# Kernel tuning notes

Hardware: AMD Instinct MI355X
Metric: run time of the kernel (lower is better)

## Reference

```python
import jax, jax.numpy as jnp
import numpy as np

INPUT_SIZE = 2048
HIDDEN_SIZE = 2048
BATCH = 4096


def setup_inputs() -> dict:
    key = jax.random.key(0)
    ks = jax.random.split(key, 12)
    std = 1.0 / HIDDEN_SIZE ** 0.5
    def u(k, shape):
        return jax.random.uniform(k, shape, jnp.float32, -std, std)
    inp = {
        "x": jax.random.normal(ks[0], (BATCH, INPUT_SIZE), jnp.float32),
        "h": jax.random.normal(ks[1], (BATCH, HIDDEN_SIZE), jnp.float32),
        "c": jax.random.normal(ks[2], (BATCH, HIDDEN_SIZE), jnp.float32),
        "weight_ii": u(ks[3], (HIDDEN_SIZE, INPUT_SIZE)),
        "weight_if": u(ks[4], (HIDDEN_SIZE, INPUT_SIZE)),
        "weight_ig": u(ks[5], (HIDDEN_SIZE, INPUT_SIZE)),
        "weight_io": u(ks[6], (HIDDEN_SIZE, INPUT_SIZE)),
        "weight_hi": u(ks[7], (HIDDEN_SIZE, HIDDEN_SIZE)),
        "weight_hf": u(ks[8], (HIDDEN_SIZE, HIDDEN_SIZE)),
        "weight_hg": u(ks[9], (HIDDEN_SIZE, HIDDEN_SIZE)),
        "weight_ho": u(ks[10], (HIDDEN_SIZE, HIDDEN_SIZE)),
        "bias_i": u(ks[11], (HIDDEN_SIZE,)),
        "bias_f": u(jax.random.fold_in(key, 100), (HIDDEN_SIZE,)),
        "bias_g": u(jax.random.fold_in(key, 101), (HIDDEN_SIZE,)),
        "bias_o": u(jax.random.fold_in(key, 102), (HIDDEN_SIZE,)),
    }
    return inp


def reference(x, h, c, weight_ii, weight_if, weight_ig, weight_io,
              weight_hi, weight_hf, weight_hg, weight_ho,
              bias_i, bias_f, bias_g, bias_o):
    # Fuse the 4 input projections and 4 hidden projections into 2 GEMMs
    # (same math as 8 separate matmuls in the original module).
    W_x = jnp.concatenate([weight_ii, weight_if, weight_ig, weight_io], axis=0)  # [4H, I]
    W_h = jnp.concatenate([weight_hi, weight_hf, weight_hg, weight_ho], axis=0)  # [4H, H]
    b = jnp.concatenate([bias_i, bias_f, bias_g, bias_o], axis=0)                # [4H]
    gates = x @ W_x.T + h @ W_h.T + b                                            # [B, 4H]
    gi, gf, gg, go = jnp.split(gates, 4, axis=1)
    i = jax.nn.sigmoid(gi)
    f = jax.nn.sigmoid(gf)
    g = jnp.tanh(gg)
    o = jax.nn.sigmoid(go)
    c_new = f * c + i * g
    h_new = o * jnp.tanh(c_new)
    return (h_new, c_new)
```

## Files before the change

kernel.cpp:

```cpp
#include <hip/hip_runtime.h>
#include <cstdint>
#include <cstddef>

#define BATCH 4096
#define HID   2048
#define NT    64

typedef __attribute__((ext_vector_type(8))) short bf16x8;
typedef __attribute__((ext_vector_type(4))) float f32x4;

__device__ __forceinline__ unsigned short f2bf(float f) {
  union { float f; unsigned u; } a; a.f = f;
  unsigned u = a.u;
  return (unsigned short)((u + 0x7FFFu + ((u >> 16) & 1u)) >> 16);
}

__device__ __forceinline__ void gload_lds16(const void* g, void* l) {
  __builtin_amdgcn_global_load_lds((const __attribute__((address_space(1))) void*)g,
                                   (__attribute__((address_space(3))) void*)l, 16, 0, 0);
}

#define SCHED0() __builtin_amdgcn_sched_barrier(0)
#define SBAR()  do { SCHED0(); __builtin_amdgcn_s_barrier(); SCHED0(); } while (0)
#define WAITV(N) do { SCHED0(); asm volatile("s_waitcnt vmcnt(" #N ")" ::: "memory"); SCHED0(); } while (0)
#define WAITL(N) do { SCHED0(); asm volatile("s_waitcnt lgkmcnt(" #N ")" ::: "memory"); SCHED0(); } while (0)
#define DSR(dst, adr, IMM) asm volatile("ds_read_b128 %0, %1 offset:" #IMM : "=v"(dst) : "v"(adr))

#define RD_A2_LO(ADR) do { DSR(a2[0],ADR,4096); DSR(a2[1],ADR,5120); DSR(a2[2],ADR,6144); DSR(a2[3],ADR,7168); } while (0)
#define RD_A2_HI(ADR) do { DSR(a2[0],ADR,36864); DSR(a2[1],ADR,37888); DSR(a2[2],ADR,38912); DSR(a2[3],ADR,39936); } while (0)
#define RD_N_LO(AADR,BADR,A1,BF) do { \
  DSR(A1[0],AADR,0); DSR(A1[1],AADR,1024); DSR(A1[2],AADR,2048); DSR(A1[3],AADR,3072); \
  DSR(BF[0],BADR,0); DSR(BF[1],BADR,1024); DSR(BF[2],BADR,2048); DSR(BF[3],BADR,3072); } while (0)
#define RD_N_HI(AADR,BADR,A1,BF) do { \
  DSR(A1[0],AADR,32768); DSR(A1[1],AADR,33792); DSR(A1[2],AADR,34816); DSR(A1[3],AADR,35840); \
  DSR(BF[0],BADR,32768); DSR(BF[1],BADR,33792); DSR(BF[2],BADR,34816); DSR(BF[3],BADR,35840); } while (0)

#define MFMA_LO(A1, BF) do { _Pragma("unroll") \
  for (int m_ = 0; m_ < 4; m_++) { _Pragma("unroll") \
    for (int n_ = 0; n_ < 4; n_++) \
      acc[m_][n_] = __builtin_amdgcn_mfma_f32_16x16x32_bf16(A1[m_], BF[n_], acc[m_][n_], 0, 0, 0); } } while (0)
#define MFMA_HI(BF) do { _Pragma("unroll") \
  for (int m_ = 0; m_ < 4; m_++) { _Pragma("unroll") \
    for (int n_ = 0; n_ < 4; n_++) \
      acc[4+m_][n_] = __builtin_amdgcn_mfma_f32_16x16x32_bf16(a2[m_], BF[n_], acc[4+m_][n_], 0, 0, 0); } } while (0)

#define STAGE_G(KOFF, DOF) do { \
  gload_lds16(pA + (KOFF), dA + (DOF)); \
  gload_lds16(pA + 128*4096 + (KOFF), dA + (DOF) + 8192); \
  gload_lds16(pB + (KOFF), dA + (DOF) + 16384); \
  gload_lds16(pB + 32*4096 + (KOFF), dA + (DOF) + 16384 + 8192); } while (0)

#define SLOT(TOPV, RDA2CALL, RDNCALL, STAGECALL, MA1, MBF) do { \
  TOPV; SBAR(); WAITL(0); \
  RDA2CALL; \
  RDNCALL; \
  STAGECALL; \
  SCHED0(); \
  __builtin_amdgcn_s_setprio(1); MFMA_LO(MA1, MBF); __builtin_amdgcn_s_setprio(0); \
  WAITL(8); \
  __builtin_amdgcn_s_setprio(1); MFMA_HI(MBF); __builtin_amdgcn_s_setprio(0); \
} while (0)

__global__ __launch_bounds__(256) void convert_kernel(
    const float* __restrict__ x, const float* __restrict__ h,
    const float* __restrict__ wii, const float* __restrict__ wif,
    const float* __restrict__ wig, const float* __restrict__ wio,
    const float* __restrict__ whi, const float* __restrict__ whf,
    const float* __restrict__ whg, const float* __restrict__ who,
    unsigned short* __restrict__ Abf, unsigned short* __restrict__ Wbf) {
  int seg = blockIdx.y;
  const float* src;
  unsigned short* dst;
  int ofs;
  size_t rofs;
  if (seg < 4) {
    src = (seg < 2) ? x : h;
    dst = Abf;
    ofs = (seg < 2) ? 0 : 2048;
    rofs = (seg & 1) ? 2048 : 0;
    src += rofs * 2048;
  } else {
    int g = (seg - 4) & 3;
    dst = Wbf + (size_t)g * 2048 * 4096;
    ofs = (seg >= 8) ? 2048 : 0;
    rofs = 0;
    switch (seg) {
      case 4: src = wii; break; case 5: src = wif; break;
      case 6: src = wig; break; case 7: src = wio; break;
      case 8: src = whi; break; case 9: src = whf; break;
      case 10: src = whg; break; default: src = who; break;
    }
  }
  size_t idx = (size_t)blockIdx.x * 256 + threadIdx.x;
  size_t e = idx * 4;
  int n = (int)(e >> 11);
  int k = (int)(e & 2047);
  float4 v = *(const float4*)(src + e);
  ushort4 o;
  o.x = f2bf(v.x); o.y = f2bf(v.y); o.z = f2bf(v.z); o.w = f2bf(v.w);
  *(ushort4*)(dst + (rofs + (size_t)n) * 4096 + ofs + k) = o;
}

__global__ __launch_bounds__(512, 2) void lstm_gemm8(
    const unsigned short* __restrict__ Abf, const unsigned short* __restrict__ Wbf,
    const float* __restrict__ c_in,
    const float* __restrict__ bias_i, const float* __restrict__ bias_f,
    const float* __restrict__ bias_g, const float* __restrict__ bias_o,
    float* __restrict__ out) {
  __shared__ unsigned short lds[2][4][256 * 32];

  int tid = threadIdx.x;
  int lane = tid & 63;
  int wid = tid >> 6;
  int wr = wid >> 2;
  int wc = wid & 3;
  int lrow = lane & 15;
  int qh = lane >> 4;

  int bid = blockIdx.x;
  int xcd = bid & 7;
  int t7 = bid >> 3;
  int mt = t7 & 15;
  int bn = xcd * 4 + (t7 >> 4);
  int m0 = mt * 256;

  int r0 = tid >> 2, cc0 = tid & 3;
  int ccs0 = cc0 ^ ((r0 >> 1) & 3);
  const unsigned short* pA = Abf + (size_t)(m0 + r0) * 4096 + ccs0 * 8;
  int g0 = (r0 >> 4) & 3;
  int jw = bn * 64 + ((r0 >> 6) & 3) * 16 + (r0 & 15);
  const unsigned short* pB = Wbf + ((size_t)g0 * 2048 + jw) * 4096 + ccs0 * 8;

  char* L0 = (char*)&lds[0][0][0];
  char* dA = L0 + tid * 16;
  unsigned ldsOff = (unsigned)(size_t)(__attribute__((address_space(3))) char*)L0;

  int arow0 = wr * 128 + lrow;
  int brow0 = wc * 64 + lrow;
  unsigned qsA = ((unsigned)(qh ^ ((arow0 >> 1) & 3))) << 4;
  unsigned qsB = ((unsigned)(qh ^ ((brow0 >> 1) & 3))) << 4;
  unsigned a0 = ldsOff + (unsigned)arow0 * 64 + qsA;
  unsigned b0 = ldsOff + 16384u + (unsigned)brow0 * 64 + qsB;
  unsigned a1v = a0 + 65536u;
  unsigned b1v = b0 + 65536u;

  f32x4 acc[8][4];
  #pragma unroll
  for (int a = 0; a < 8; a++)
    #pragma unroll
    for (int b = 0; b < 4; b++) acc[a][b] = (f32x4){0.f, 0.f, 0.f, 0.f};

  bf16x8 a1A[4], bfA[4], a1B[4], bfB[4], a2[4];

  STAGE_G(0, 0);
  STAGE_G(32, 32768);
  STAGE_G(64, 65536);
  WAITV(8);
  SBAR();
  RD_N_LO(a0, b0, a1A, bfA);

  for (int i = 0; i < 31; ++i) {
    int kb = i * 128;
    SLOT(WAITV(4), RD_A2_LO(a0), RD_N_HI(a0, b0, a1B, bfB), STAGE_G(kb + 96, 98304), a1A, bfA);
    SLOT(WAITV(4), RD_A2_HI(a0), RD_N_LO(a1v, b1v, a1A, bfA), STAGE_G(kb + 128, 0), a1B, bfB);
    SLOT(WAITV(4), RD_A2_LO(a1v), RD_N_HI(a1v, b1v, a1B, bfB), STAGE_G(kb + 160, 32768), a1A, bfA);
    SLOT(WAITV(4), RD_A2_HI(a1v), RD_N_LO(a0, b0, a1A, bfA), STAGE_G(kb + 192, 65536), a1B, bfB);
  }

  SLOT(WAITV(4), RD_A2_LO(a0), RD_N_HI(a0, b0, a1B, bfB), STAGE_G(4064, 98304), a1A, bfA);
  SLOT(WAITV(4), RD_A2_HI(a0), RD_N_LO(a1v, b1v, a1A, bfA), (void)0, a1B, bfB);
  SLOT(WAITV(0), RD_A2_LO(a1v), RD_N_HI(a1v, b1v, a1B, bfB), (void)0, a1A, bfA);
  WAITL(0);
  RD_A2_HI(a1v);
  SCHED0();
  __builtin_amdgcn_s_setprio(1); MFMA_LO(a1B, bfB); __builtin_amdgcn_s_setprio(0);
  WAITL(0);
  __builtin_amdgcn_s_setprio(1); MFMA_HI(bfB); __builtin_amdgcn_s_setprio(0);

  int j = bn * 64 + wc * 16 + lrow;
  float bi = bias_i[j], bff = bias_f[j], bgg = bias_g[j], bo = bias_o[j];
  int rbase = m0 + wr * 128 + qh * 4;
  #pragma unroll
  for (int mf = 0; mf < 8; mf++) {
    #pragma unroll
    for (int qq = 0; qq < 4; qq++) {
      int m = rbase + mf * 16 + qq;
      size_t off = (size_t)m * HID + j;
      float gi = acc[mf][0][qq] + bi;
      float gf = acc[mf][1][qq] + bff;
      float gg = acc[mf][2][qq] + bgg;
      float go = acc[mf][3][qq] + bo;
      float iv = 1.f / (1.f + __expf(-gi));
      float fv = 1.f / (1.f + __expf(-gf));
      float gv = tanhf(gg);
      float ov = 1.f / (1.f + __expf(-go));
      float cn = fv * c_in[off] + iv * gv;
      float hn = ov * tanhf(cn);
      out[off] = hn;
      out[(size_t)BATCH * HID + off] = cn;
    }
  }
}

__global__ __launch_bounds__(256) void lstm_gemm_fb(
    const float* __restrict__ x, const float* __restrict__ h,
    const float* __restrict__ wii, const float* __restrict__ wif,
    const float* __restrict__ wig, const float* __restrict__ wio,
    const float* __restrict__ whi, const float* __restrict__ whf,
    const float* __restrict__ whg, const float* __restrict__ who,
    const float* __restrict__ c_in,
    const float* __restrict__ bias_i, const float* __restrict__ bias_f,
    const float* __restrict__ bias_g, const float* __restrict__ bias_o,
    float* __restrict__ out) {
  __shared__ unsigned short Ald[128 * 64];
  __shared__ unsigned short Bld[128 * 64];
  int tid = threadIdx.x;
  int lane = tid & 63;
  int wid = tid >> 6;
  int wr = wid >> 1, wc = wid & 1;
  int bid = blockIdx.x;
  int swz = (bid & 7) * 256 + (bid >> 3);
  int mt = swz & 31;
  int ht = swz >> 5;
  int m0 = mt * 128;
  int j0 = ht * 32;
  f32x4 acc[4][4];
  #pragma unroll
  for (int a = 0; a < 4; a++)
    #pragma unroll
    for (int b = 0; b < 4; b++) acc[a][b] = (f32x4){0.f, 0.f, 0.f, 0.f};
  int lrow = lane & 15;
  int lsw = lrow & 7;
  int qbase = lane >> 4;
  for (int kt = 0; kt < 64; kt++) {
    int k0 = kt * 64;
    const float* Asrc = (k0 < 2048) ? x : h;
    int ka = k0 & 2047;
    #pragma unroll
    for (int i = 0; i < 4; i++) {
      int c = i * 256 + tid;
      int r = c >> 3, cc = c & 7;
      int ccs = cc ^ (r & 7);
      const float* s = Asrc + (size_t)(m0 + r) * 2048 + ka + ccs * 8;
      float4 v0 = *(const float4*)s;
      float4 v1 = *(const float4*)(s + 4);
      bf16x8 pk;
      pk[0] = (short)f2bf(v0.x); pk[1] = (short)f2bf(v0.y);
      pk[2] = (short)f2bf(v0.z); pk[3] = (short)f2bf(v0.w);
      pk[4] = (short)f2bf(v1.x); pk[5] = (short)f2bf(v1.y);
      pk[6] = (short)f2bf(v1.z); pk[7] = (short)f2bf(v1.w);
      *(bf16x8*)((char*)Ald + (size_t)c * 16) = pk;
    }
    #pragma unroll
    for (int i = 0; i < 4; i++) {
      int c = i * 256 + tid;
      int rb = c >> 3, cc = c & 7;
      int ccs = cc ^ (rb & 7);
      int g = rb >> 5, jj = rb & 31;
      const float* Bsrc;
      if (k0 < 2048) Bsrc = (g == 0) ? wii : (g == 1) ? wif : (g == 2) ? wig : wio;
      else           Bsrc = (g == 0) ? whi : (g == 1) ? whf : (g == 2) ? whg : who;
      const float* s = Bsrc + (size_t)(j0 + jj) * 2048 + ka + ccs * 8;
      float4 v0 = *(const float4*)s;
      float4 v1 = *(const float4*)(s + 4);
      bf16x8 pk;
      pk[0] = (short)f2bf(v0.x); pk[1] = (short)f2bf(v0.y);
      pk[2] = (short)f2bf(v0.z); pk[3] = (short)f2bf(v0.w);
      pk[4] = (short)f2bf(v1.x); pk[5] = (short)f2bf(v1.y);
      pk[6] = (short)f2bf(v1.z); pk[7] = (short)f2bf(v1.w);
      *(bf16x8*)((char*)Bld + (size_t)c * 16) = pk;
    }
    __syncthreads();
    #pragma unroll
    for (int ks = 0; ks < 2; ks++) {
      int q = ks * 4 + qbase;
      int qs8 = (q ^ lsw) * 8;
      bf16x8 af[4], bg[4];
      #pragma unroll
      for (int mf = 0; mf < 4; mf++)
        af[mf] = *(const bf16x8*)&Ald[(wr * 64 + mf * 16 + lrow) * 64 + qs8];
      #pragma unroll
      for (int g = 0; g < 4; g++)
        bg[g] = *(const bf16x8*)&Bld[(g * 32 + wc * 16 + lrow) * 64 + qs8];
      #pragma unroll
      for (int mf = 0; mf < 4; mf++)
        #pragma unroll
        for (int g = 0; g < 4; g++)
          acc[mf][g] = __builtin_amdgcn_mfma_f32_16x16x32_bf16(af[mf], bg[g], acc[mf][g], 0, 0, 0);
    }
    __syncthreads();
  }
  int j = j0 + wc * 16 + lrow;
  float bi = bias_i[j], bff = bias_f[j], bgg = bias_g[j], bo = bias_o[j];
  int rbase = m0 + wr * 64 + (lane >> 4) * 4;
  #pragma unroll
  for (int mf = 0; mf < 4; mf++) {
    #pragma unroll
    for (int q = 0; q < 4; q++) {
      int m = rbase + mf * 16 + q;
      size_t off = (size_t)m * HID + j;
      float gi = acc[mf][0][q] + bi;
      float gf = acc[mf][1][q] + bff;
      float gg = acc[mf][2][q] + bgg;
      float go = acc[mf][3][q] + bo;
      float iv = 1.f / (1.f + __expf(-gi));
      float fv = 1.f / (1.f + __expf(-gf));
      float gv = tanhf(gg);
      float ov = 1.f / (1.f + __expf(-go));
      float cn = fv * c_in[off] + iv * gv;
      float hn = ov * tanhf(cn);
      out[off] = hn;
      out[(size_t)BATCH * HID + off] = cn;
    }
  }
}

extern "C" void kernel_launch(void* const* d_in, const int* in_sizes, int n_in,
                              void* d_out, int out_size, void* d_ws, size_t ws_size,
                              hipStream_t stream) {
  const float* x   = (const float*)d_in[0];
  const float* h   = (const float*)d_in[1];
  const float* c   = (const float*)d_in[2];
  const float* wii = (const float*)d_in[3];
  const float* wif = (const float*)d_in[4];
  const float* wig = (const float*)d_in[5];
  const float* wio = (const float*)d_in[6];
  const float* whi = (const float*)d_in[7];
  const float* whf = (const float*)d_in[8];
  const float* whg = (const float*)d_in[9];
  const float* who = (const float*)d_in[10];
  const float* bi  = (const float*)d_in[11];
  const float* bf  = (const float*)d_in[12];
  const float* bg  = (const float*)d_in[13];
  const float* bo  = (const float*)d_in[14];
  float* out = (float*)d_out;

  size_t needA = (size_t)4096 * 4096 * 2;
  size_t needW = (size_t)8192 * 4096 * 2;

  if (ws_size >= needA + needW) {
    unsigned short* Abf = (unsigned short*)d_ws;
    unsigned short* Wbf = (unsigned short*)((char*)d_ws + needA);
    convert_kernel<<<dim3(4096, 12), 256, 0, stream>>>(
        x, h, wii, wif, wig, wio, whi, whf, whg, who, Abf, Wbf);
    lstm_gemm8<<<512, 512, 0, stream>>>(Abf, Wbf, c, bi, bf, bg, bo, out);
  } else {
    lstm_gemm_fb<<<2048, 256, 0, stream>>>(
        x, h, wii, wif, wig, wio, whi, whf, whg, who,
        c, bi, bf, bg, bo, out);
  }
}
```

Measured before the change: 315.7 us.

## Deepen LDS pipeline to five rotating stages with runtime offset ring

Replaces the fixed two-buffer, hi/lo-halved LDS layout with a five-slot ring buffer of 32 KB stages whose offsets rotate at runtime. Four K-chunks are prefetched up front, and each slot now waits with a looser vmcnt, so more global loads are in flight during the MFMA work. The cost is more LDS (160 KB), which may reduce occupancy below two blocks per CU. Runtime offset arithmetic also replaces the immediate-offset addressing, adding extra scalar and vector ALU work.

After: 321.2 us. Within noise of the previous version (+1.7%).

```diff
diff --git a/kernel.cpp b/kernel.cpp
--- a/kernel.cpp
+++ b/kernel.cpp
@@ -4,7 +4,6 @@
 
 #define BATCH 4096
 #define HID   2048
-#define NT    64
 
 typedef __attribute__((ext_vector_type(8))) short bf16x8;
 typedef __attribute__((ext_vector_type(4))) float f32x4;
@@ -26,14 +25,10 @@
 #define WAITL(N) do { SCHED0(); asm volatile("s_waitcnt lgkmcnt(" #N ")" ::: "memory"); SCHED0(); } while (0)
 #define DSR(dst, adr, IMM) asm volatile("ds_read_b128 %0, %1 offset:" #IMM : "=v"(dst) : "v"(adr))
 
-#define RD_A2_LO(ADR) do { DSR(a2[0],ADR,4096); DSR(a2[1],ADR,5120); DSR(a2[2],ADR,6144); DSR(a2[3],ADR,7168); } while (0)
-#define RD_A2_HI(ADR) do { DSR(a2[0],ADR,36864); DSR(a2[1],ADR,37888); DSR(a2[2],ADR,38912); DSR(a2[3],ADR,39936); } while (0)
-#define RD_N_LO(AADR,BADR,A1,BF) do { \
+#define RD_A2(ADR) do { DSR(a2[0],ADR,4096); DSR(a2[1],ADR,5120); DSR(a2[2],ADR,6144); DSR(a2[3],ADR,7168); } while (0)
+#define RD_N(AADR,BADR,A1,BF) do { \
   DSR(A1[0],AADR,0); DSR(A1[1],AADR,1024); DSR(A1[2],AADR,2048); DSR(A1[3],AADR,3072); \
   DSR(BF[0],BADR,0); DSR(BF[1],BADR,1024); DSR(BF[2],BADR,2048); DSR(BF[3],BADR,3072); } while (0)
-#define RD_N_HI(AADR,BADR,A1,BF) do { \
-  DSR(A1[0],AADR,32768); DSR(A1[1],AADR,33792); DSR(A1[2],AADR,34816); DSR(A1[3],AADR,35840); \
-  DSR(BF[0],BADR,32768); DSR(BF[1],BADR,33792); DSR(BF[2],BADR,34816); DSR(BF[3],BADR,35840); } while (0)
 
 #define MFMA_LO(A1, BF) do { _Pragma("unroll") \
   for (int m_ = 0; m_ < 4; m_++) { _Pragma("unroll") \
@@ -48,17 +43,21 @@
   gload_lds16(pA + (KOFF), dA + (DOF)); \
   gload_lds16(pA + 128*4096 + (KOFF), dA + (DOF) + 8192); \
   gload_lds16(pB + (KOFF), dA + (DOF) + 16384); \
-  gload_lds16(pB + 32*4096 + (KOFF), dA + (DOF) + 16384 + 8192); } while (0)
-
-#define SLOT(TOPV, RDA2CALL, RDNCALL, STAGECALL, MA1, MBF) do { \
-  TOPV; SBAR(); WAITL(0); \
-  RDA2CALL; \
-  RDNCALL; \
-  STAGECALL; \
-  SCHED0(); \
+  gload_lds16(pB + 32*4096 + (KOFF), dA + (DOF) + 24576); } while (0)
+
+#define ADVR(o) do { (o) += 32768; if ((o) == 163840) (o) = 0; } while (0)
+
+#define SLOT(VN, SA, SB, STG, MA1, MBF) do { \
+  WAITV(VN); \
+  SBAR(); \
+  { unsigned aC_ = aBase + (unsigned)o_c; RD_A2(aC_); } \
+  { unsigned aN_ = aBase + (unsigned)o_n, bN_ = bBase + (unsigned)o_n; RD_N(aN_, bN_, SA, SB); } \
+  STG; \
+  WAITL(12); \
   __builtin_amdgcn_s_setprio(1); MFMA_LO(MA1, MBF); __builtin_amdgcn_s_setprio(0); \
   WAITL(8); \
   __builtin_amdgcn_s_setprio(1); MFMA_HI(MBF); __builtin_amdgcn_s_setprio(0); \
+  ADVR(o_c); ADVR(o_n); ADVR(o_s); koff += 32; \
 } while (0)
 
 __global__ __launch_bounds__(256) void convert_kernel(
@@ -107,7 +106,7 @@
     const float* __restrict__ bias_i, const float* __restrict__ bias_f,
     const float* __restrict__ bias_g, const float* __restrict__ bias_o,
     float* __restrict__ out) {
-  __shared__ unsigned short lds[2][4][256 * 32];
+  __shared__ unsigned short lds[5 * 16384];
 
   int tid = threadIdx.x;
   int lane = tid & 63;
@@ -131,7 +130,7 @@
   int jw = bn * 64 + ((r0 >> 6) & 3) * 16 + (r0 & 15);
   const unsigned short* pB = Wbf + ((size_t)g0 * 2048 + jw) * 4096 + ccs0 * 8;
 
-  char* L0 = (char*)&lds[0][0][0];
+  char* L0 = (char*)&lds[0];
   char* dA = L0 + tid * 16;
   unsigned ldsOff = (unsigned)(size_t)(__attribute__((address_space(3))) char*)L0;
 
@@ -139,10 +138,8 @@
   int brow0 = wc * 64 + lrow;
   unsigned qsA = ((unsigned)(qh ^ ((arow0 >> 1) & 3))) << 4;
   unsigned qsB = ((unsigned)(qh ^ ((brow0 >> 1) & 3))) << 4;
-  unsigned a0 = ldsOff + (unsigned)arow0 * 64 + qsA;
-  unsigned b0 = ldsOff + 16384u + (unsigned)brow0 * 64 + qsB;
-  unsigned a1v = a0 + 65536u;
-  unsigned b1v = b0 + 65536u;
+  unsigned aBase = ldsOff + (unsigned)arow0 * 64 + qsA;
+  unsigned bBase = ldsOff + 16384u + (unsigned)brow0 * 64 + qsB;
 
   f32x4 acc[8][4];
   #pragma unroll
@@ -152,30 +149,33 @@
 
   bf16x8 a1A[4], bfA[4], a1B[4], bfB[4], a2[4];
 
+  int o_c = 0, o_n = 32768, o_s = 131072;
+  int koff = 128;
+
   STAGE_G(0, 0);
   STAGE_G(32, 32768);
   STAGE_G(64, 65536);
-  WAITV(8);
+  STAGE_G(96, 98304);
+  WAITV(12);
   SBAR();
-  RD_N_LO(a0, b0, a1A, bfA);
-
-  for (int i = 0; i < 31; ++i) {
-    int kb = i * 128;
-    SLOT(WAITV(4), RD_A2_LO(a0), RD_N_HI(a0, b0, a1B, bfB), STAGE_G(kb + 96, 98304), a1A, bfA);
-    SLOT(WAITV(4), RD_A2_HI(a0), RD_N_LO(a1v, b1v, a1A, bfA), STAGE_G(kb + 128, 0), a1B, bfB);
-    SLOT(WAITV(4), RD_A2_LO(a1v), RD_N_HI(a1v, b1v, a1B, bfB), STAGE_G(kb + 160, 32768), a1A, bfA);
-    SLOT(WAITV(4), RD_A2_HI(a1v), RD_N_LO(a0, b0, a1A, bfA), STAGE_G(kb + 192, 65536), a1B, bfB);
-  }
-
-  SLOT(WAITV(4), RD_A2_LO(a0), RD_N_HI(a0, b0, a1B, bfB), STAGE_G(4064, 98304), a1A, bfA);
-  SLOT(WAITV(4), RD_A2_HI(a0), RD_N_LO(a1v, b1v, a1A, bfA), (void)0, a1B, bfB);
-  SLOT(WAITV(0), RD_A2_LO(a1v), RD_N_HI(a1v, b1v, a1B, bfB), (void)0, a1A, bfA);
-  WAITL(0);
-  RD_A2_HI(a1v);
-  SCHED0();
-  __builtin_amdgcn_s_setprio(1); MFMA_LO(a1B, bfB); __builtin_amdgcn_s_setprio(0);
-  WAITL(0);
-  __builtin_amdgcn_s_setprio(1); MFMA_HI(bfB); __builtin_amdgcn_s_setprio(0);
+  { unsigned aN_ = aBase, bN_ = bBase; RD_N(aN_, bN_, a1A, bfA); }
+
+  for (int i = 0; i < 62; ++i) {
+    SLOT(8, a1B, bfB, STAGE_G(koff, o_s), a1A, bfA);
+    SLOT(8, a1A, bfA, STAGE_G(koff, o_s), a1B, bfB);
+  }
+
+  SLOT(8, a1B, bfB, (void)0, a1A, bfA);
+  SLOT(4, a1A, bfA, (void)0, a1B, bfB);
+  SLOT(0, a1B, bfB, (void)0, a1A, bfA);
+  {
+    unsigned aC_ = aBase + (unsigned)o_c;
+    RD_A2(aC_);
+    WAITL(4);
+    __builtin_amdgcn_s_setprio(1); MFMA_LO(a1B, bfB); __builtin_amdgcn_s_setprio(0);
+    WAITL(0);
+    __builtin_amdgcn_s_setprio(1); MFMA_HI(bfB); __builtin_amdgcn_s_setprio(0);
+  }
 
   int j = bn * 64 + wc * 16 + lrow;
   float bi = bias_i[j], bff = bias_f[j], bgg = bias_g[j], bo = bias_o[j];
```
